# Kernel optimization log

Measured on AMD Instinct MI355X. Metric: run time of the kernel, lower is better.

## Reference

```python
import jax, jax.numpy as jnp
import numpy as np

N, E, IN, OUT, H = 100000, 1600000, 128, 128, 4
C = OUT // H
NEG_SLOPE = 0.2  # PyG GATConv default LeakyReLU slope
BN_EPS = 1e-5


def setup_inputs() -> dict:
    key = jax.random.key(0)
    k = jax.random.split(key, 6)
    x = jax.random.normal(k[0], (N, IN), dtype=jnp.float32)
    edge_index = jax.random.randint(k[1], (2, E), 0, N, dtype=jnp.int64)
    W = jax.random.normal(k[2], (IN, H * C), dtype=jnp.float32) / np.sqrt(IN)
    att_src = jax.random.normal(k[3], (H, C), dtype=jnp.float32) * 0.1
    att_dst = jax.random.normal(k[4], (H, C), dtype=jnp.float32) * 0.1
    gat_bias = jnp.zeros((H * C,), dtype=jnp.float32)
    bn_gamma = jnp.ones((OUT,), dtype=jnp.float32)
    bn_beta = jnp.zeros((OUT,), dtype=jnp.float32)
    return {"x": x, "edge_index": edge_index, "W": W, "att_src": att_src,
            "att_dst": att_dst, "gat_bias": gat_bias, "bn_gamma": bn_gamma,
            "bn_beta": bn_beta}


def reference(x, edge_index, W, att_src, att_dst, gat_bias, bn_gamma, bn_beta):
    n = x.shape[0]
    # GATConv: linear transform, per-head view [N,H,C]
    h = (x @ W).reshape(n, H, C)
    # add self loops (PyG default add_self_loops=True)
    loop = jnp.arange(n, dtype=edge_index.dtype)
    src = jnp.concatenate([edge_index[0], loop])  # message source j
    dst = jnp.concatenate([edge_index[1], loop])  # message target i
    # per-node attention logits [N,H]
    a_src = jnp.einsum('nhc,hc->nh', h, att_src)
    a_dst = jnp.einsum('nhc,hc->nh', h, att_dst)
    # per-edge logits [Etot,H], LeakyReLU, segment softmax over dst
    e = jax.nn.leaky_relu(a_src[src] + a_dst[dst], NEG_SLOPE)
    m = jax.ops.segment_max(e, dst, num_segments=n)
    e = jnp.exp(e - m[dst])
    s = jax.ops.segment_sum(e, dst, num_segments=n)
    alpha = e / (s[dst] + 1e-16)  # dropout(p=0.3) is identity at eval
    # weighted scatter-add aggregation
    msg = h[src] * alpha[:, :, None]  # [Etot,H,C]
    out = jax.ops.segment_sum(msg, dst, num_segments=n).reshape(n, H * C)
    out = out + gat_bias
    # BatchNorm1d (batch statistics, biased var)
    mean = jnp.mean(out, axis=0)
    var = jnp.var(out, axis=0)
    out = bn_gamma * (out - mean) * jax.lax.rsqrt(var + BN_EPS) + bn_beta
    # residual (proj is Identity since in_ch == out_ch) + ReLU
    return jax.nn.relu(out + x)
```

## Files before the change

### kernel.cpp

```cpp
#include <hip/hip_runtime.h>

#define NEG 0.2f
#define EPB 8192
#define NB64MAX 1568
#define CAPB_MAX 1536
#define REPL 16

typedef short short8 __attribute__((ext_vector_type(8)));
typedef float floatx4 __attribute__((ext_vector_type(4)));

__device__ __forceinline__ float bf_lo(unsigned int u) { return __uint_as_float(u << 16); }
__device__ __forceinline__ float bf_hi(unsigned int u) { return __uint_as_float(u & 0xffff0000u); }
__device__ __forceinline__ unsigned short f2bf(float f) {
    unsigned int u = __float_as_uint(f);
    return (unsigned short)((u + 0x7fff + ((u >> 16) & 1)) >> 16);
}

__global__ __launch_bounds__(256) void k_wconv(const float* __restrict__ W,
                                               unsigned short* __restrict__ Wtb,
                                               int* __restrict__ gcur,
                                               float* __restrict__ gsum,
                                               float* __restrict__ gsumsq, int NB) {
    int i = blockIdx.x * 256 + threadIdx.x;
    int n = i >> 7, k = i & 127;
    Wtb[n * 128 + k] = f2bf(W[k * 128 + n]);
    if (i < NB) gcur[i] = 0;
    if (i < REPL * 128) { gsum[i] = 0.f; gsumsq[i] = 0.f; }
}

__global__ __launch_bounds__(256) void k_gemm(const float* __restrict__ x,
                                              const unsigned short* __restrict__ Wtb,
                                              const float* __restrict__ att_src,
                                              const float* __restrict__ att_dst,
                                              unsigned short* __restrict__ hb,
                                              unsigned int* __restrict__ asd, int N) {
    __shared__ unsigned short As[64 * 128];
    __shared__ unsigned short Bs[128 * 128];
    int t = threadIdx.x;
    int r0 = blockIdx.x * 64;
#pragma unroll
    for (int p = 0; p < 8; p++) {
        int idx = t + 256 * p;
        int row = idx >> 5, c4 = idx & 31;
        float4 v = make_float4(0.f, 0.f, 0.f, 0.f);
        if (r0 + row < N) v = *(const float4*)&x[(size_t)(r0 + row) * 128 + c4 * 4];
        int kb = c4 >> 1;
        uint2* d = (uint2*)&As[row * 128 + ((kb ^ (row & 7)) << 3) + (c4 & 1) * 4];
        uint2 pk;
        pk.x = ((unsigned int)f2bf(v.y) << 16) | f2bf(v.x);
        pk.y = ((unsigned int)f2bf(v.w) << 16) | f2bf(v.z);
        *d = pk;
    }
#pragma unroll
    for (int p = 0; p < 8; p++) {
        int idx = t + 256 * p;
        int n = idx >> 4, k8 = idx & 15;
        *(short8*)&Bs[n * 128 + ((k8 ^ (n & 7)) << 3)] = *(const short8*)&Wtb[n * 128 + k8 * 8];
    }
    __syncthreads();
    int lane = t & 63, wv = t >> 6;
    int m16 = lane & 15, quad = lane >> 4;
    int rowbase = wv * 16;
    floatx4 acc[8];
#pragma unroll
    for (int c = 0; c < 8; c++) acc[c] = (floatx4){0.f, 0.f, 0.f, 0.f};
#pragma unroll
    for (int ks = 0; ks < 4; ks++) {
        int arow = rowbase + m16;
        short8 a = *(const short8*)&As[arow * 128 + (((ks * 4 + quad) ^ (arow & 7)) << 3)];
#pragma unroll
        for (int c = 0; c < 8; c++) {
            int brow = c * 16 + m16;
            short8 b = *(const short8*)&Bs[brow * 128 + (((ks * 4 + quad) ^ (brow & 7)) << 3)];
            acc[c] = __builtin_amdgcn_mfma_f32_16x16x32_bf16(a, b, acc[c], 0, 0, 0);
        }
    }
    float ps[4][4], pd[4][4];
#pragma unroll
    for (int hd = 0; hd < 4; hd++)
#pragma unroll
        for (int r = 0; r < 4; r++) { ps[hd][r] = 0.f; pd[hd][r] = 0.f; }
#pragma unroll
    for (int c = 0; c < 8; c++) {
        int col = c * 16 + m16;
        float as_ = att_src[col], ad_ = att_dst[col];
        int hd = c >> 1;
#pragma unroll
        for (int r = 0; r < 4; r++) {
            float v = acc[c][r];
            int row = r0 + rowbase + quad * 4 + r;
            if (row < N) hb[(size_t)row * 128 + col] = f2bf(v);
            ps[hd][r] = fmaf(v, as_, ps[hd][r]);
            pd[hd][r] = fmaf(v, ad_, pd[hd][r]);
        }
    }
#pragma unroll
    for (int off = 1; off < 16; off <<= 1) {
#pragma unroll
        for (int hd = 0; hd < 4; hd++)
#pragma unroll
            for (int r = 0; r < 4; r++) {
                ps[hd][r] += __shfl_xor(ps[hd][r], off, 16);
                pd[hd][r] += __shfl_xor(pd[hd][r], off, 16);
            }
    }
    if (m16 == 0) {
#pragma unroll
        for (int r = 0; r < 4; r++) {
            int row = r0 + rowbase + quad * 4 + r;
            if (row < N)
#pragma unroll
                for (int hd = 0; hd < 4; hd++)
                    asd[row * 4 + hd] = ((unsigned int)f2bf(pd[hd][r]) << 16) | f2bf(ps[hd][r]);
        }
    }
}

__global__ __launch_bounds__(512) void k_bin3(const int* __restrict__ ei,
                                              int* __restrict__ gcur,
                                              unsigned int* __restrict__ pairs,
                                              int E, int NB, int CAPB) {
    __shared__ unsigned int sorted[EPB];
    __shared__ unsigned short bkt[EPB];
    __shared__ int cnt[NB64MAX];
    __shared__ int A[NB64MAX];
    __shared__ int wsum[8];
    int t = threadIdx.x;
    for (int i = t; i < NB; i += 512) cnt[i] = 0;
    __syncthreads();
    int base = blockIdx.x * EPB, end = min(base + EPB, E);
    int nLoc = end - base;
    unsigned int pay[16];
    unsigned short bk[16];
#pragma unroll
    for (int q = 0; q < 16; q++) {
        int i = base + t + q * 512;
        unsigned int p = 0xFFFFFFFFu;
        int b = 0;
        if (i < end) {
            int s = ei[i], d = ei[E + i];
            p = (unsigned int)s | ((unsigned int)(d & 63) << 20);
            b = d >> 6;
            atomicAdd(&cnt[b], 1);
        }
        pay[q] = p;
        bk[q] = (unsigned short)b;
    }
    __syncthreads();
    int b0 = 4 * t;
    int c0 = 0, c1 = 0, c2 = 0, c3 = 0;
    if (b0 < NB)     c0 = cnt[b0];
    if (b0 + 1 < NB) c1 = cnt[b0 + 1];
    if (b0 + 2 < NB) c2 = cnt[b0 + 2];
    if (b0 + 3 < NB) c3 = cnt[b0 + 3];
    int local = c0 + c1 + c2 + c3;
    int lane = t & 63, wv = t >> 6;
    int scan = local;
#pragma unroll
    for (int off = 1; off < 64; off <<= 1) {
        int v = __shfl_up(scan, off, 64);
        if (lane >= off) scan += v;
    }
    if (lane == 63) wsum[wv] = scan;
    __syncthreads();
    int woff = 0;
    for (int w = 0; w < wv; w++) woff += wsum[w];
    int lst = woff + scan - local;
    if (b0 < NB) {
        int s = c0 ? atomicAdd(&gcur[b0], c0) : 0;
        A[b0] = (s + c0 <= CAPB) ? (b0 * CAPB + s - lst) : INT_MIN;
        cnt[b0] = lst + c0; lst += c0;
    }
    if (b0 + 1 < NB) {
        int s = c1 ? atomicAdd(&gcur[b0 + 1], c1) : 0;
        A[b0 + 1] = (s + c1 <= CAPB) ? ((b0 + 1) * CAPB + s - lst) : INT_MIN;
        cnt[b0 + 1] = lst + c1; lst += c1;
    }
    if (b0 + 2 < NB) {
        int s = c2 ? atomicAdd(&gcur[b0 + 2], c2) : 0;
        A[b0 + 2] = (s + c2 <= CAPB) ? ((b0 + 2) * CAPB + s - lst) : INT_MIN;
        cnt[b0 + 2] = lst + c2; lst += c2;
    }
    if (b0 + 3 < NB) {
        int s = c3 ? atomicAdd(&gcur[b0 + 3], c3) : 0;
        A[b0 + 3] = (s + c3 <= CAPB) ? ((b0 + 3) * CAPB + s - lst) : INT_MIN;
        cnt[b0 + 3] = lst + c3;
    }
    __syncthreads();
#pragma unroll
    for (int q = 0; q < 16; q++) {
        if (pay[q] != 0xFFFFFFFFu) {
            int b = bk[q];
            int pos = atomicSub(&cnt[b], 1) - 1;
            sorted[pos] = pay[q];
            bkt[pos] = (unsigned short)b;
        }
    }
    __syncthreads();
    for (int i = t; i < nLoc; i += 512) {
        int b = bkt[i];
        int a = A[b];
        if (a != INT_MIN) pairs[(size_t)(a + i)] = sorted[i];
    }
}

__global__ __launch_bounds__(256) void k_agg2(const unsigned int* __restrict__ hb,
                                              const unsigned int* __restrict__ asd,
                                              const int* __restrict__ gcur,
                                              const unsigned int* __restrict__ pairs,
                                              unsigned int* __restrict__ yb,
                                              float* __restrict__ gsum,
                                              float* __restrict__ gsumsq,
                                              int N, int CAPB) {
    __shared__ unsigned int ent[CAPB_MAX];
    __shared__ float red[1024];
    __shared__ int cnt64[64], off64[64], cur64[64], stmp[64];
    int b = blockIdx.x, t = threadIdx.x;
    size_t base = (size_t)b * CAPB;
    int cnt = min(gcur[b], CAPB);
    if (t < 64) cnt64[t] = 0;
    __syncthreads();
    unsigned int pe[6];
#pragma unroll
    for (int q = 0; q < 6; q++) {
        int i = t + q * 256;
        unsigned int e = 0xFFFFFFFFu;
        if (i < cnt) {
            e = pairs[base + i];
            atomicAdd(&cnt64[(e >> 20) & 63], 1);
        }
        pe[q] = e;
    }
    __syncthreads();
    if (t < 64) stmp[t] = cnt64[t];
    __syncthreads();
    for (int d = 1; d < 64; d <<= 1) {
        int add = (t < 64 && t >= d) ? stmp[t - d] : 0;
        __syncthreads();
        if (t < 64) stmp[t] += add;
        __syncthreads();
    }
    if (t < 64) { int ex = stmp[t] - cnt64[t]; off64[t] = ex; cur64[t] = ex; }
    __syncthreads();
#pragma unroll
    for (int q = 0; q < 6; q++) {
        unsigned int e = pe[q];
        if (e != 0xFFFFFFFFu) {
            int slot = atomicAdd(&cur64[(e >> 20) & 63], 1);
            ent[slot] = e & 0xFFFFFu;
        }
    }
    __syncthreads();
    int lane = t & 63, wv = t >> 6;
    int head = lane >> 4, sub = lane & 15, wsel = lane & 48;
    float t_sl = 0.f, t_sh = 0.f, t_ql = 0.f, t_qh = 0.f;
    for (int k = 0; k < 16; k++) {
        int ln = wv * 16 + k;
        int n = b * 64 + ln;
        if (n >= N) break;
        unsigned int au = asd[n * 4 + head];
        float adst = bf_hi(au);
        float e0 = bf_lo(au) + adst;
        e0 = e0 > 0.f ? e0 : NEG * e0;
        float w0 = __expf(e0);
        unsigned int hu = hb[(size_t)n * 64 + lane];
        float acc0 = w0 * bf_lo(hu), acc1 = w0 * bf_hi(hu), sw = w0;
        int st = off64[ln], c = cnt64[ln];
        int sjn = n;
        float evn = 0.f;
        if (sub < c) {
            sjn = (int)ent[st + sub];
            evn = bf_lo(asd[sjn * 4 + head]);
        }
        for (int eb = 0; eb < c; eb += 16) {
            int sj_l = sjn;
            float ev = evn + adst;
            ev = ev > 0.f ? ev : NEG * ev;
            float wl = (eb + sub < c) ? __expf(ev) : 0.f;
            if (eb + 16 + sub < c) {
                sjn = (int)ent[st + eb + 16 + sub];
                evn = bf_lo(asd[sjn * 4 + head]);
            } else sjn = n;
#pragma unroll
            for (int j = 0; j < 16; j++) {
                int sj = __shfl(sj_l, j, 64);
                float wj = __shfl(wl, wsel | j, 64);
                unsigned int hj = hb[(size_t)sj * 64 + lane];
                acc0 = fmaf(wj, bf_lo(hj), acc0);
                acc1 = fmaf(wj, bf_hi(hj), acc1);
                sw += wj;
            }
        }
        float inv = 1.0f / (sw + 1e-16f);
        unsigned int yw = ((unsigned int)f2bf(acc1 * inv) << 16) | f2bf(acc0 * inv);
        yb[(size_t)n * 64 + lane] = yw;
        float ylo = bf_lo(yw), yhi = bf_hi(yw);
        t_sl += ylo; t_sh += yhi;
        t_ql = fmaf(ylo, ylo, t_ql);
        t_qh = fmaf(yhi, yhi, t_qh);
    }
    red[t] = t_sl; red[256 + t] = t_sh; red[512 + t] = t_ql; red[768 + t] = t_qh;
    __syncthreads();
    if (t < 64) {
        float a = red[t] + red[t + 64] + red[t + 128] + red[t + 192];
        float bb = red[256 + t] + red[256 + t + 64] + red[256 + t + 128] + red[256 + t + 192];
        float cc = red[512 + t] + red[512 + t + 64] + red[512 + t + 128] + red[512 + t + 192];
        float dd = red[768 + t] + red[768 + t + 64] + red[768 + t + 128] + red[768 + t + 192];
        int rep = (b & (REPL - 1)) * 128;
        atomicAdd(&gsum[rep + 2 * t], a);
        atomicAdd(&gsum[rep + 2 * t + 1], bb);
        atomicAdd(&gsumsq[rep + 2 * t], cc);
        atomicAdd(&gsumsq[rep + 2 * t + 1], dd);
    }
}

__global__ __launch_bounds__(256) void k_final(const unsigned int* __restrict__ yb,
                                               const float* __restrict__ x,
                                               const float* __restrict__ gsum,
                                               const float* __restrict__ gsumsq,
                                               const float* __restrict__ gamma,
                                               const float* __restrict__ beta,
                                               float* __restrict__ out, int N, int total4) {
    __shared__ float scS[128], shS[128];
    int t = threadIdx.x;
    if (t < 128) {
        float s = 0.f, q = 0.f;
#pragma unroll
        for (int r = 0; r < REPL; r++) {
            s += gsum[r * 128 + t];
            q += gsumsq[r * 128 + t];
        }
        float invN = 1.0f / (float)N;
        float mean = s * invN;
        float var = q * invN - mean * mean;
        float sc = gamma[t] * rsqrtf(var + 1e-5f);
        scS[t] = sc;
        shS[t] = beta[t] - mean * sc;
    }
    __syncthreads();
    int i = blockIdx.x * 256 + t;
    if (i >= total4) return;
    int c4 = i & 31;
    uint2 u = ((const uint2*)yb)[i];
    float4 xv = ((const float4*)x)[i];
    float4 r;
    r.x = fmaxf(fmaf(bf_lo(u.x), scS[c4 * 4 + 0], shS[c4 * 4 + 0]) + xv.x, 0.f);
    r.y = fmaxf(fmaf(bf_hi(u.x), scS[c4 * 4 + 1], shS[c4 * 4 + 1]) + xv.y, 0.f);
    r.z = fmaxf(fmaf(bf_lo(u.y), scS[c4 * 4 + 2], shS[c4 * 4 + 2]) + xv.z, 0.f);
    r.w = fmaxf(fmaf(bf_hi(u.y), scS[c4 * 4 + 3], shS[c4 * 4 + 3]) + xv.w, 0.f);
    ((float4*)out)[i] = r;
}

extern "C" void kernel_launch(void* const* d_in, const int* in_sizes, int n_in,
                              void* d_out, int out_size, void* d_ws, size_t ws_size,
                              hipStream_t stream) {
    const float* x       = (const float*)d_in[0];
    const int*   ei      = (const int*)d_in[1];
    const float* W       = (const float*)d_in[2];
    const float* att_src = (const float*)d_in[3];
    const float* att_dst = (const float*)d_in[4];
    const float* gamma   = (const float*)d_in[6];
    const float* beta    = (const float*)d_in[7];
    int N = in_sizes[0] / 128;
    int E = in_sizes[1] / 2;
    int NB = (N + 63) / 64;

    char* base = (char*)d_ws;
    size_t off = 0;
    auto alloc = [&](size_t b) -> char* {
        char* p = base + off;
        off = (off + b + 255) & ~(size_t)255;
        return p;
    };
    unsigned short* hb  = (unsigned short*)alloc((size_t)N * 128 * 2);
    unsigned int*   yb  = (unsigned int*)alloc((size_t)N * 64 * 4);
    unsigned int*   asd = (unsigned int*)alloc((size_t)N * 4 * 4);
    unsigned short* Wtb = (unsigned short*)alloc(128 * 128 * 2);
    int*   gcur   = (int*)alloc((size_t)NB * 4);
    float* gsum   = (float*)alloc(REPL * 128 * 4);
    float* gsumsq = (float*)alloc(REPL * 128 * 4);
    size_t rem = (ws_size > off) ? (ws_size - off) : 0;
    int CAPB = (int)((rem / ((size_t)NB * 4)) & ~(size_t)15);
    if (CAPB > CAPB_MAX) CAPB = CAPB_MAX;
    unsigned int* pairs = (unsigned int*)alloc((size_t)NB * CAPB * 4);
    float* outp = (float*)d_out;

    int chunks = (E + EPB - 1) / EPB;
    k_wconv<<<64, 256, 0, stream>>>(W, Wtb, gcur, gsum, gsumsq, NB);
    k_gemm<<<(N + 63) / 64, 256, 0, stream>>>(x, Wtb, att_src, att_dst, hb, asd, N);
    k_bin3<<<chunks, 512, 0, stream>>>(ei, gcur, pairs, E, NB, CAPB);
    k_agg2<<<NB, 256, 0, stream>>>((const unsigned int*)hb, asd, gcur, pairs, yb,
                                   gsum, gsumsq, N, CAPB);
    k_final<<<(N * 32 + 255) / 256, 256, 0, stream>>>(yb, x, gsum, gsumsq, gamma, beta,
                                                      outp, N, N * 32);
}
```

Before: 278.2 us.

## Stage GEMM bf16 output through LDS for coalesced stores; precompute BN scale/shift once

The GEMM epilogue now writes the bf16 results into a padded shared-memory tile and then stores them to global memory with 16-byte vectorized, row-contiguous writes, instead of scattered 2-byte stores. Separately, BatchNorm scale and shift are computed once by a tiny one-block kernel rather than redundantly in every block of the final kernel. This adds an extra kernel launch and two extra block barriers in exchange for fewer and better-coalesced global transactions.

```diff
diff --git a/kernel.cpp b/kernel.cpp
--- a/kernel.cpp
+++ b/kernel.cpp
@@ -88,8 +88,6 @@
 #pragma unroll
         for (int r = 0; r < 4; r++) {
             float v = acc[c][r];
-            int row = r0 + rowbase + quad * 4 + r;
-            if (row < N) hb[(size_t)row * 128 + col] = f2bf(v);
             ps[hd][r] = fmaf(v, as_, ps[hd][r]);
             pd[hd][r] = fmaf(v, ad_, pd[hd][r]);
         }
@@ -112,6 +110,28 @@
 #pragma unroll
                 for (int hd = 0; hd < 4; hd++)
                     asd[row * 4 + hd] = ((unsigned int)f2bf(pd[hd][r]) << 16) | f2bf(ps[hd][r]);
+        }
+    }
+    __syncthreads();
+    unsigned short* Cb = Bs;
+#pragma unroll
+    for (int c = 0; c < 8; c++) {
+        int col = c * 16 + m16;
+#pragma unroll
+        for (int r = 0; r < 4; r++) {
+            int lrow = rowbase + quad * 4 + r;
+            Cb[lrow * 136 + col] = f2bf(acc[c][r]);
+        }
+    }
+    __syncthreads();
+#pragma unroll
+    for (int p = 0; p < 4; p++) {
+        int idx = t + 256 * p;
+        int lrow = idx >> 4, seg = idx & 15;
+        int row = r0 + lrow;
+        if (row < N) {
+            uint4 v = *(const uint4*)&Cb[lrow * 136 + seg * 8];
+            *(uint4*)&hb[(size_t)row * 128 + seg * 8] = v;
         }
     }
 }
@@ -314,29 +334,35 @@
     }
 }
 
+__global__ __launch_bounds__(128) void k_bnfinal(const float* __restrict__ gsum,
+                                                 const float* __restrict__ gsumsq,
+                                                 const float* __restrict__ gamma,
+                                                 const float* __restrict__ beta,
+                                                 float* __restrict__ scale,
+                                                 float* __restrict__ shift, int N) {
+    int c = threadIdx.x;
+    float s = 0.f, q = 0.f;
+#pragma unroll
+    for (int r = 0; r < REPL; r++) {
+        s += gsum[r * 128 + c];
+        q += gsumsq[r * 128 + c];
+    }
+    float invN = 1.0f / (float)N;
+    float mean = s * invN;
+    float var = q * invN - mean * mean;
+    float sc = gamma[c] * rsqrtf(var + 1e-5f);
+    scale[c] = sc;
+    shift[c] = beta[c] - mean * sc;
+}
+
 __global__ __launch_bounds__(256) void k_final(const unsigned int* __restrict__ yb,
                                                const float* __restrict__ x,
-                                               const float* __restrict__ gsum,
-                                               const float* __restrict__ gsumsq,
-                                               const float* __restrict__ gamma,
-                                               const float* __restrict__ beta,
-                                               float* __restrict__ out, int N, int total4) {
+                                               const float* __restrict__ scale,
+                                               const float* __restrict__ shift,
+                                               float* __restrict__ out, int total4) {
     __shared__ float scS[128], shS[128];
     int t = threadIdx.x;
-    if (t < 128) {
-        float s = 0.f, q = 0.f;
-#pragma unroll
-        for (int r = 0; r < REPL; r++) {
-            s += gsum[r * 128 + t];
-            q += gsumsq[r * 128 + t];
-        }
-        float invN = 1.0f / (float)N;
-        float mean = s * invN;
-        float var = q * invN - mean * mean;
-        float sc = gamma[t] * rsqrtf(var + 1e-5f);
-        scS[t] = sc;
-        shS[t] = beta[t] - mean * sc;
-    }
+    if (t < 128) { scS[t] = scale[t]; shS[t] = shift[t]; }
     __syncthreads();
     int i = blockIdx.x * 256 + t;
     if (i >= total4) return;
@@ -379,6 +405,8 @@
     int*   gcur   = (int*)alloc((size_t)NB * 4);
     float* gsum   = (float*)alloc(REPL * 128 * 4);
     float* gsumsq = (float*)alloc(REPL * 128 * 4);
+    float* scale  = (float*)alloc(512);
+    float* shift  = (float*)alloc(512);
     size_t rem = (ws_size > off) ? (ws_size - off) : 0;
     int CAPB = (int)((rem / ((size_t)NB * 4)) & ~(size_t)15);
     if (CAPB > CAPB_MAX) CAPB = CAPB_MAX;
@@ -391,6 +419,6 @@
     k_bin3<<<chunks, 512, 0, stream>>>(ei, gcur, pairs, E, NB, CAPB);
     k_agg2<<<NB, 256, 0, stream>>>((const unsigned int*)hb, asd, gcur, pairs, yb,
                                    gsum, gsumsq, N, CAPB);
-    k_final<<<(N * 32 + 255) / 256, 256, 0, stream>>>(yb, x, gsum, gsumsq, gamma, beta,
-                                                      outp, N, N * 32);
-}
+    k_bnfinal<<<1, 128, 0, stream>>>(gsum, gsumsq, gamma, beta, scale, shift, N);
+    k_final<<<(N * 32 + 255) / 256, 256, 0, stream>>>(yb, x, scale, shift, outp, N * 32);
+}
```

Measured after the change: 273.4 us. No clear change (-1.7%).

## Fuse edge binning and GEMM into one launch with staged hb stores

Applied to the files above, without the earlier changes.

Merges the edge-binning kernel and the projection GEMM into a single kernel: the first blocks bin the edges (now 256 threads, 32 edges per thread, 7 buckets per thread for the scan) and the remaining blocks run the GEMM. This lets the two independent stages overlap on the GPU and saves a launch. The GEMM epilogue now writes the bf16 output through a padded shared-memory tile so global stores are coalesced 16-byte writes instead of scattered 2-byte ones. In exchange, the shared-memory footprint becomes the maximum of the two stages (about 60KB), which can lower occupancy for the GEMM blocks. The binning blocks also carry more registers per thread.

```diff
diff --git a/kernel.cpp b/kernel.cpp
--- a/kernel.cpp
+++ b/kernel.cpp
@@ -28,16 +28,98 @@
     if (i < REPL * 128) { gsum[i] = 0.f; gsumsq[i] = 0.f; }
 }
 
-__global__ __launch_bounds__(256) void k_gemm(const float* __restrict__ x,
-                                              const unsigned short* __restrict__ Wtb,
-                                              const float* __restrict__ att_src,
-                                              const float* __restrict__ att_dst,
-                                              unsigned short* __restrict__ hb,
-                                              unsigned int* __restrict__ asd, int N) {
-    __shared__ unsigned short As[64 * 128];
-    __shared__ unsigned short Bs[128 * 128];
+__global__ __launch_bounds__(256) void k_gb(const float* __restrict__ x,
+                                            const unsigned short* __restrict__ Wtb,
+                                            const float* __restrict__ att_src,
+                                            const float* __restrict__ att_dst,
+                                            unsigned short* __restrict__ hb,
+                                            unsigned int* __restrict__ asd,
+                                            const int* __restrict__ ei,
+                                            int* __restrict__ gcur,
+                                            unsigned int* __restrict__ pairs,
+                                            int N, int E, int NB, int CAPB, int chunks) {
+    __shared__ __align__(16) char smem[61840];
     int t = threadIdx.x;
-    int r0 = blockIdx.x * 64;
+    if ((int)blockIdx.x < chunks) {
+        unsigned int* sorted = (unsigned int*)smem;
+        unsigned short* bkt  = (unsigned short*)(smem + 32768);
+        int* cnt             = (int*)(smem + 49152);
+        int* A               = (int*)(smem + 55424);
+        int* wsum            = (int*)(smem + 61696);
+        for (int i = t; i < NB; i += 256) cnt[i] = 0;
+        __syncthreads();
+        int base = blockIdx.x * EPB, end = min(base + EPB, E);
+        int nLoc = end - base;
+        unsigned int pay[32];
+        unsigned short bk[32];
+#pragma unroll
+        for (int q = 0; q < 32; q++) {
+            int i = base + t + q * 256;
+            unsigned int p = 0xFFFFFFFFu;
+            int b = 0;
+            if (i < end) {
+                int s = ei[i], d = ei[E + i];
+                p = (unsigned int)s | ((unsigned int)(d & 63) << 20);
+                b = d >> 6;
+                atomicAdd(&cnt[b], 1);
+            }
+            pay[q] = p;
+            bk[q] = (unsigned short)b;
+        }
+        __syncthreads();
+        int b0 = 7 * t;
+        int cl[7];
+        int local = 0;
+#pragma unroll
+        for (int j = 0; j < 7; j++) {
+            int b = b0 + j;
+            cl[j] = (b < NB) ? cnt[b] : 0;
+            local += cl[j];
+        }
+        int lane = t & 63, wv = t >> 6;
+        int scan = local;
+#pragma unroll
+        for (int off = 1; off < 64; off <<= 1) {
+            int v = __shfl_up(scan, off, 64);
+            if (lane >= off) scan += v;
+        }
+        if (lane == 63) wsum[wv] = scan;
+        __syncthreads();
+        int woff = 0;
+        for (int w = 0; w < wv; w++) woff += wsum[w];
+        int lst = woff + scan - local;
+#pragma unroll
+        for (int j = 0; j < 7; j++) {
+            int b = b0 + j;
+            if (b < NB) {
+                int c = cl[j];
+                int s = c ? atomicAdd(&gcur[b], c) : 0;
+                A[b] = (s + c <= CAPB) ? (b * CAPB + s - lst) : INT_MIN;
+                cnt[b] = lst + c;
+                lst += c;
+            }
+        }
+        __syncthreads();
+#pragma unroll
+        for (int q = 0; q < 32; q++) {
+            if (pay[q] != 0xFFFFFFFFu) {
+                int b = bk[q];
+                int pos = atomicSub(&cnt[b], 1) - 1;
+                sorted[pos] = pay[q];
+                bkt[pos] = (unsigned short)b;
+            }
+        }
+        __syncthreads();
+        for (int i = t; i < nLoc; i += 256) {
+            int b = bkt[i];
+            int a = A[b];
+            if (a != INT_MIN) pairs[(size_t)(a + i)] = sorted[i];
+        }
+        return;
+    }
+    unsigned short* As = (unsigned short*)smem;
+    unsigned short* Bs = (unsigned short*)(smem + 16384);
+    int r0 = ((int)blockIdx.x - chunks) * 64;
 #pragma unroll
     for (int p = 0; p < 8; p++) {
         int idx = t + 256 * p;
@@ -88,8 +170,6 @@
 #pragma unroll
         for (int r = 0; r < 4; r++) {
             float v = acc[c][r];
-            int row = r0 + rowbase + quad * 4 + r;
-            if (row < N) hb[(size_t)row * 128 + col] = f2bf(v);
             ps[hd][r] = fmaf(v, as_, ps[hd][r]);
             pd[hd][r] = fmaf(v, ad_, pd[hd][r]);
         }
@@ -114,93 +194,27 @@
                     asd[row * 4 + hd] = ((unsigned int)f2bf(pd[hd][r]) << 16) | f2bf(ps[hd][r]);
         }
     }
-}
-
-__global__ __launch_bounds__(512) void k_bin3(const int* __restrict__ ei,
-                                              int* __restrict__ gcur,
-                                              unsigned int* __restrict__ pairs,
-                                              int E, int NB, int CAPB) {
-    __shared__ unsigned int sorted[EPB];
-    __shared__ unsigned short bkt[EPB];
-    __shared__ int cnt[NB64MAX];
-    __shared__ int A[NB64MAX];
-    __shared__ int wsum[8];
-    int t = threadIdx.x;
-    for (int i = t; i < NB; i += 512) cnt[i] = 0;
-    __syncthreads();
-    int base = blockIdx.x * EPB, end = min(base + EPB, E);
-    int nLoc = end - base;
-    unsigned int pay[16];
-    unsigned short bk[16];
-#pragma unroll
-    for (int q = 0; q < 16; q++) {
-        int i = base + t + q * 512;
-        unsigned int p = 0xFFFFFFFFu;
-        int b = 0;
-        if (i < end) {
-            int s = ei[i], d = ei[E + i];
-            p = (unsigned int)s | ((unsigned int)(d & 63) << 20);
-            b = d >> 6;
-            atomicAdd(&cnt[b], 1);
-        }
-        pay[q] = p;
-        bk[q] = (unsigned short)b;
-    }
-    __syncthreads();
-    int b0 = 4 * t;
-    int c0 = 0, c1 = 0, c2 = 0, c3 = 0;
-    if (b0 < NB)     c0 = cnt[b0];
-    if (b0 + 1 < NB) c1 = cnt[b0 + 1];
-    if (b0 + 2 < NB) c2 = cnt[b0 + 2];
-    if (b0 + 3 < NB) c3 = cnt[b0 + 3];
-    int local = c0 + c1 + c2 + c3;
-    int lane = t & 63, wv = t >> 6;
-    int scan = local;
-#pragma unroll
-    for (int off = 1; off < 64; off <<= 1) {
-        int v = __shfl_up(scan, off, 64);
-        if (lane >= off) scan += v;
-    }
-    if (lane == 63) wsum[wv] = scan;
-    __syncthreads();
-    int woff = 0;
-    for (int w = 0; w < wv; w++) woff += wsum[w];
-    int lst = woff + scan - local;
-    if (b0 < NB) {
-        int s = c0 ? atomicAdd(&gcur[b0], c0) : 0;
-        A[b0] = (s + c0 <= CAPB) ? (b0 * CAPB + s - lst) : INT_MIN;
-        cnt[b0] = lst + c0; lst += c0;
-    }
-    if (b0 + 1 < NB) {
-        int s = c1 ? atomicAdd(&gcur[b0 + 1], c1) : 0;
-        A[b0 + 1] = (s + c1 <= CAPB) ? ((b0 + 1) * CAPB + s - lst) : INT_MIN;
-        cnt[b0 + 1] = lst + c1; lst += c1;
-    }
-    if (b0 + 2 < NB) {
-        int s = c2 ? atomicAdd(&gcur[b0 + 2], c2) : 0;
-        A[b0 + 2] = (s + c2 <= CAPB) ? ((b0 + 2) * CAPB + s - lst) : INT_MIN;
-        cnt[b0 + 2] = lst + c2; lst += c2;
-    }
-    if (b0 + 3 < NB) {
-        int s = c3 ? atomicAdd(&gcur[b0 + 3], c3) : 0;
-        A[b0 + 3] = (s + c3 <= CAPB) ? ((b0 + 3) * CAPB + s - lst) : INT_MIN;
-        cnt[b0 + 3] = lst + c3;
-    }
-    __syncthreads();
-#pragma unroll
-    for (int q = 0; q < 16; q++) {
-        if (pay[q] != 0xFFFFFFFFu) {
-            int b = bk[q];
-            int pos = atomicSub(&cnt[b], 1) - 1;
-            sorted[pos] = pay[q];
-            bkt[pos] = (unsigned short)b;
-        }
-    }
-    __syncthreads();
-    for (int i = t; i < nLoc; i += 512) {
-        int b = bkt[i];
-        int a = A[b];
-        if (a != INT_MIN) pairs[(size_t)(a + i)] = sorted[i];
+    __syncthreads();
+    unsigned short* Cb = Bs;
+#pragma unroll
+    for (int c = 0; c < 8; c++) {
+        int col = c * 16 + m16;
+#pragma unroll
+        for (int r = 0; r < 4; r++) {
+            int lrow = rowbase + quad * 4 + r;
+            Cb[lrow * 136 + col] = f2bf(acc[c][r]);
+        }
+    }
+    __syncthreads();
+#pragma unroll
+    for (int p = 0; p < 4; p++) {
+        int idx = t + 256 * p;
+        int lrow = idx >> 4, seg = idx & 15;
+        int row = r0 + lrow;
+        if (row < N) {
+            uint4 v = *(const uint4*)&Cb[lrow * 136 + seg * 8];
+            *(uint4*)&hb[(size_t)row * 128 + seg * 8] = v;
+        }
     }
 }
 
@@ -386,9 +400,10 @@
     float* outp = (float*)d_out;
 
     int chunks = (E + EPB - 1) / EPB;
+    int gemmB = (N + 63) / 64;
     k_wconv<<<64, 256, 0, stream>>>(W, Wtb, gcur, gsum, gsumsq, NB);
-    k_gemm<<<(N + 63) / 64, 256, 0, stream>>>(x, Wtb, att_src, att_dst, hb, asd, N);
-    k_bin3<<<chunks, 512, 0, stream>>>(ei, gcur, pairs, E, NB, CAPB);
+    k_gb<<<chunks + gemmB, 256, 0, stream>>>(x, Wtb, att_src, att_dst, hb, asd,
+                                             ei, gcur, pairs, N, E, NB, CAPB, chunks);
     k_agg2<<<NB, 256, 0, stream>>>((const unsigned int*)hb, asd, gcur, pairs, yb,
                                    gsum, gsumsq, N, CAPB);
     k_final<<<(N * 32 + 255) / 256, 256, 0, stream>>>(yb, x, gsum, gsumsq, gamma, beta,
```

Result: no change. 282.3 us (+1.4%).
